# Performance work log

Measured on AMD Instinct MI355X. Metric: run time of the kernel, lower is better.

## Reference

```python
import jax, jax.numpy as jnp
import numpy as np

B, H, W, D = 2, 64, 64, 512
D_HEAD = 64
N_HEADS = D // D_HEAD
KERNEL = 7


def make_neighbourhood_mask(kernel: int, canvas_h: int, canvas_w: int) -> jnp.ndarray:
    """Boolean [HW, HW] mask: query (i,j) attends to a clamped kernel x kernel window."""
    h_ramp = jnp.arange(canvas_h)
    w_ramp = jnp.arange(canvas_w)
    h_pos, w_pos = jnp.meshgrid(h_ramp, w_ramp, indexing='ij')
    start_h = jnp.clip(h_pos - kernel // 2, 0, canvas_h - kernel)[..., None, None]
    end_h = start_h + kernel
    start_w = jnp.clip(w_pos - kernel // 2, 0, canvas_w - kernel)[..., None, None]
    end_w = start_w + kernel
    h_range = h_ramp.reshape(1, 1, canvas_h, 1)
    w_range = w_ramp.reshape(1, 1, 1, canvas_w)
    mask = (h_range >= start_h) & (h_range < end_h) & (w_range >= start_w) & (w_range < end_w)
    return mask.reshape(canvas_h * canvas_w, canvas_h * canvas_w)


def setup_inputs() -> dict:
    key = jax.random.key(0)
    k1, k2, k3 = jax.random.split(key, 3)
    x = jax.random.normal(k1, (B, H, W, D), dtype=jnp.float32)
    w_qkv = jax.random.normal(k2, (3 * D, D), dtype=jnp.float32) * (D ** -0.5)
    w_out = jax.random.normal(k3, (D, D), dtype=jnp.float32) * (D ** -0.5)
    return {"x": x, "w_qkv": w_qkv, "w_out": w_out}


def reference(x, w_qkv, w_out):
    b, h, w, d = x.shape
    s = h * w
    # qkv projection (Linear, no bias): [b,h,w,3d]
    qkv = jnp.einsum('bhwd,ed->bhwe', x, w_qkv)
    # split per torch rearrange 'n h w (t nh e) -> t n nh (h w) e'
    qkv = qkv.reshape(b, s, 3, N_HEADS, D_HEAD).transpose(2, 0, 3, 1, 4)  # [3,b,nh,s,e]
    q, k, v = qkv[0], qkv[1], qkv[2]
    mask = make_neighbourhood_mask(KERNEL, h, w)  # [s, s] bool
    scale = D_HEAD ** -0.5
    scores = jnp.einsum('bnse,bnte->bnst', q, k) * scale  # [b,nh,s,s]
    neg_inf = jnp.finfo(scores.dtype).min
    scores = jnp.where(mask[None, None, :, :], scores, neg_inf)
    attn = jax.nn.softmax(scores, axis=-1)
    out = jnp.einsum('bnst,bnte->bnse', attn, v)  # [b,nh,s,e]
    out = out.transpose(0, 2, 1, 3).reshape(b, h, w, d)  # [b,h,w,d]
    return jnp.einsum('bhwd,ed->bhwe', out, w_out)
```

## Files before the change

### kernel.cpp

```cpp
#include <hip/hip_runtime.h>
#include <hip/hip_bf16.h>


typedef __bf16 bf16x8 __attribute__((ext_vector_type(8)));
typedef __bf16 bf16x4 __attribute__((ext_vector_type(4)));
typedef float  f32x4  __attribute__((ext_vector_type(4)));

__global__ __launch_bounds__(256) void cvt_all(
    const float* __restrict__ x, const float* __restrict__ wq,
    const float* __restrict__ wo, __bf16* __restrict__ xb,
    __bf16* __restrict__ wqb, __bf16* __restrict__ wob) {
  int i = blockIdx.x * 256 + threadIdx.x;
  const float* src;
  __bf16* dst;
  int j = i;
  if (j < 1048576) {
    src = x; dst = xb;
  } else if (j < 1048576 + 196608) {
    j -= 1048576; src = wq; dst = wqb;
  } else {
    j -= 1048576 + 196608; src = wo; dst = wob;
  }
  f32x4 v = ((const f32x4*)src)[j];
  bf16x4 o;
  o[0] = (__bf16)v[0]; o[1] = (__bf16)v[1];
  o[2] = (__bf16)v[2]; o[3] = (__bf16)v[3];
  ((bf16x4*)dst)[j] = o;
}

__device__ __forceinline__ void gload_lds16(const __bf16* g, __bf16* l) {
  __builtin_amdgcn_global_load_lds(
      (const __attribute__((address_space(1))) void*)g,
      (__attribute__((address_space(3))) void*)l, 16, 0, 0);
}

template <bool QKV, int BN>
__global__ __launch_bounds__(256, 3) void gemm_lds(
    const __bf16* __restrict__ A, const __bf16* __restrict__ W,
    __bf16* __restrict__ qo, __bf16* __restrict__ ko, __bf16* __restrict__ vo,
    float* __restrict__ co, int etiles) {
  constexpr int K = 512;
  constexpr int NT = BN / 32;
  __shared__ alignas(16) __bf16 Al[128 * 32];
  __shared__ alignas(16) __bf16 Wl[BN * 32];
  const int tid = threadIdx.x;
  const int wv = tid >> 6, lane = tid & 63;
  const int n16 = lane & 15, quad = lane >> 4;
  const int bi = blockIdx.x / etiles, be = blockIdx.x % etiles;
  const int i0 = bi << 7, e0 = be * BN;
  const int wm = (wv & 1) << 6, we = (wv >> 1) * (BN / 2);

  const int srow = (wv << 4) + (lane >> 2);
  const int scol = (lane & 3) << 3;
  const __bf16* gA = A + (size_t)(i0 + srow) * K + scol;
  const __bf16* gW = W + (size_t)(e0 + srow) * K + scol;
  __bf16* lA = &Al[(wv << 9) + (lane << 3)];
  __bf16* lW = &Wl[(wv << 9) + (lane << 3)];

  f32x4 acc[4][NT];
#pragma unroll
  for (int a = 0; a < 4; ++a)
#pragma unroll
    for (int b = 0; b < NT; ++b) acc[a][b] = (f32x4){0.f, 0.f, 0.f, 0.f};

  for (int k0 = 0; k0 < K; k0 += 32) {
    if (k0) __syncthreads();
    gload_lds16(gA + k0, lA);
    gload_lds16(gA + (size_t)64 * K + k0, lA + 64 * 32);
    gload_lds16(gW + k0, lW);
    if (BN == 128) gload_lds16(gW + (size_t)64 * K + k0, lW + 64 * 32);
    __syncthreads();

    bf16x8 af[4], wf[NT];
#pragma unroll
    for (int t = 0; t < 4; ++t)
      af[t] = *(const bf16x8*)&Al[(wm + t * 16 + n16) * 32 + quad * 8];
#pragma unroll
    for (int t = 0; t < NT; ++t)
      wf[t] = *(const bf16x8*)&Wl[(we + t * 16 + n16) * 32 + quad * 8];
#pragma unroll
    for (int mt = 0; mt < 4; ++mt)
#pragma unroll
      for (int nt = 0; nt < NT; ++nt)
        acc[mt][nt] = __builtin_amdgcn_mfma_f32_16x16x32_bf16(
            af[mt], wf[nt], acc[mt][nt], 0, 0, 0);
  }

#pragma unroll
  for (int mt = 0; mt < 4; ++mt)
#pragma unroll
    for (int nt = 0; nt < NT; ++nt) {
      f32x4 f = acc[mt][nt];
      int e = e0 + we + nt * 16 + n16;
#pragma unroll
      for (int rg = 0; rg < 4; ++rg) {
        int i = i0 + wm + mt * 16 + quad * 4 + rg;
        float val = f[rg];
        if (QKV) {
          int t = e >> 9, head = (e >> 6) & 7, dh = e & 63;
          int b = i >> 12, s = i & 4095;
          int bh = b * 8 + head;
          if (t == 2) {
            vo[((size_t)bh * 64 + dh) * 4096 + s] = (__bf16)val;
          } else {
            size_t off = (((size_t)bh * 4096) + s) * 64 + dh;
            ((t == 0) ? qo : ko)[off] = (__bf16)val;
          }
        } else {
          co[(size_t)i * 512 + e] = val;
        }
      }
    }
}

__global__ __launch_bounds__(256) void attn_mfma(
    const __bf16* __restrict__ q, const __bf16* __restrict__ k,
    const __bf16* __restrict__ vt, __bf16* __restrict__ out) {
  __shared__ alignas(16) __bf16 r1[14848];
  __shared__ alignas(16) __bf16 sbuf[4][16][232];
  const int tid = threadIdx.x;
  const int wv = tid >> 6;
  const int lane = tid & 63;
  const int n16 = lane & 15, quad = lane >> 4;
  const int bh = blockIdx.x >> 6;
  const int tile = blockIdx.x & 63;
  const int qh0 = (tile >> 3) << 3, qw0 = (tile & 7) << 3;
  int wh0 = qh0 - 3; wh0 = wh0 < 0 ? 0 : (wh0 > 50 ? 50 : wh0);
  int wc0 = qw0 - 3; wc0 = wc0 < 0 ? 0 : (wc0 > 48 ? 48 : wc0);
  wc0 &= ~1;
  const size_t base = (size_t)bh * 4096 * 64;

  const int qi_a = wv * 16 + n16;
  const int sqa = (qh0 + (qi_a >> 3)) * 64 + qw0 + (qi_a & 7);
  const __bf16* qp = q + base + (size_t)sqa * 64 + quad * 8;
  bf16x8 aq0 = *(const bf16x8*)qp;
  bf16x8 aq1 = *(const bf16x8*)(qp + 32);

  const __bf16* kbase = k + base;
#pragma unroll
  for (int i = 0; i < 7; ++i) {
    int ch = i * 256 + tid;
    int kr = ch >> 7, wi = ch & 127;
    int kc = wi >> 3, dh8 = wi & 7;
    bf16x8 d = *(const bf16x8*)(kbase +
        (size_t)((wh0 + kr) * 64 + wc0 + kc) * 64 + dh8 * 8);
    *(bf16x8*)&r1[(kr * 16 + kc) * 64 + ((dh8 ^ (kc & 7)) * 8)] = d;
  }
  __syncthreads();

  f32x4 S[14];
  const int skw = wc0 + n16;
  const int sw1 = ((quad ^ (n16 & 7)) * 8);
  const int sw2 = (((4 + quad) ^ (n16 & 7)) * 8);
#pragma unroll
  for (int nt = 0; nt < 14; ++nt) {
    int key = nt * 16 + n16;
    bf16x8 b0 = *(const bf16x8*)&r1[key * 64 + sw1];
    bf16x8 b1 = *(const bf16x8*)&r1[key * 64 + sw2];
    f32x4 s = {0.f, 0.f, 0.f, 0.f};
    s = __builtin_amdgcn_mfma_f32_16x16x32_bf16(aq0, b0, s, 0, 0, 0);
    s = __builtin_amdgcn_mfma_f32_16x16x32_bf16(aq1, b1, s, 0, 0, 0);
    S[nt] = s;
  }

  float mx[4] = {-1e30f, -1e30f, -1e30f, -1e30f};
#pragma unroll
  for (int reg = 0; reg < 4; ++reg) {
    int qi = wv * 16 + quad * 4 + reg;
    int qh = qh0 + (qi >> 3), qw = qw0 + (qi & 7);
    int sh = qh - 3; sh = sh < 0 ? 0 : (sh > 57 ? 57 : sh);
    int sw = qw - 3; sw = sw < 0 ? 0 : (sw > 57 ? 57 : sw);
    bool wok = (skw >= sw) && (skw < sw + 7);
#pragma unroll
    for (int nt = 0; nt < 14; ++nt) {
      int kh = wh0 + nt;
      bool ok = wok && (kh >= sh) && (kh < sh + 7);
      float val = ok ? S[nt][reg] * 0.125f : -1e30f;
      S[nt][reg] = val;
      mx[reg] = mx[reg] > val ? mx[reg] : val;
    }
  }
#pragma unroll
  for (int reg = 0; reg < 4; ++reg)
#pragma unroll
    for (int off = 8; off >= 1; off >>= 1) {
      float o = __shfl_xor(mx[reg], off);
      mx[reg] = mx[reg] > o ? mx[reg] : o;
    }

  float sm[4] = {0.f, 0.f, 0.f, 0.f};
#pragma unroll
  for (int nt = 0; nt < 14; ++nt)
#pragma unroll
    for (int reg = 0; reg < 4; ++reg) {
      float p = __expf(S[nt][reg] - mx[reg]);
      S[nt][reg] = p;
      sm[reg] += p;
    }
#pragma unroll
  for (int reg = 0; reg < 4; ++reg)
#pragma unroll
    for (int off = 8; off >= 1; off >>= 1) sm[reg] += __shfl_xor(sm[reg], off);

#pragma unroll
  for (int reg = 0; reg < 4; ++reg) {
    float inv = 1.f / sm[reg];
    int row = quad * 4 + reg;
#pragma unroll
    for (int nt = 0; nt < 14; ++nt)
      sbuf[wv][row][nt * 16 + n16] = (__bf16)(S[nt][reg] * inv);
  }

  __syncthreads();
  const __bf16* vtb = vt + base;
#pragma unroll
  for (int i = 0; i < 7; ++i) {
    int c = i * 256 + tid;
    int dh = c / 28, rem = c % 28;
    int kr = rem >> 1, half = rem & 1;
    bf16x8 d = *(const bf16x8*)(vtb + (size_t)dh * 4096 +
                                (wh0 + kr) * 64 + wc0 + half * 8);
    *(bf16x8*)&r1[dh * 232 + kr * 16 + half * 8] = d;
  }
  __syncthreads();

  f32x4 O[4] = {{0.f, 0.f, 0.f, 0.f},
                {0.f, 0.f, 0.f, 0.f},
                {0.f, 0.f, 0.f, 0.f},
                {0.f, 0.f, 0.f, 0.f}};
#pragma unroll
  for (int kt = 0; kt < 7; ++kt) {
    bf16x8 pa = *(const bf16x8*)&sbuf[wv][n16][kt * 32 + quad * 8];
    int key0 = kt * 32 + quad * 8;
#pragma unroll
    for (int ntv = 0; ntv < 4; ++ntv) {
      bf16x8 vb = *(const bf16x8*)&r1[(ntv * 16 + n16) * 232 + key0];
      O[ntv] = __builtin_amdgcn_mfma_f32_16x16x32_bf16(pa, vb, O[ntv], 0, 0, 0);
    }
  }

  const int b = bh >> 3, head = bh & 7;
#pragma unroll
  for (int ntv = 0; ntv < 4; ++ntv)
#pragma unroll
    for (int reg = 0; reg < 4; ++reg) {
      int qi = wv * 16 + quad * 4 + reg;
      int s_q = (qh0 + (qi >> 3)) * 64 + qw0 + (qi & 7);
      int dh = ntv * 16 + n16;
      out[((size_t)(b * 4096 + s_q)) * 512 + head * 64 + dh] =
          (__bf16)O[ntv][reg];
    }
}

extern "C" void kernel_launch(void* const* d_in, const int* in_sizes, int n_in,
                              void* d_out, int out_size, void* d_ws,
                              size_t ws_size, hipStream_t stream) {
  const float* x = (const float*)d_in[0];
  const float* w_qkv = (const float*)d_in[1];
  const float* w_out = (const float*)d_in[2];
  float* out = (float*)d_out;

  const size_t qelems = (size_t)2 * 8 * 4096 * 64;
  __bf16* q = (__bf16*)d_ws;
  __bf16* k = q + qelems;
  __bf16* vt = k + qelems;
  __bf16* xb = vt + qelems;
  __bf16* wqb = xb + qelems;
  __bf16* wob = wqb + 1536 * 512;
  __bf16* ao = xb;

  cvt_all<<<dim3(5120), dim3(256), 0, stream>>>(x, w_qkv, w_out, xb, wqb, wob);

  gemm_lds<true, 128><<<dim3(768), dim3(256), 0, stream>>>(
      xb, wqb, q, k, vt, nullptr, 12);
  attn_mfma<<<dim3(1024), dim3(256), 0, stream>>>(q, k, vt, ao);
  gemm_lds<false, 64><<<dim3(512), dim3(256), 0, stream>>>(
      ao, wob, nullptr, nullptr, nullptr, out, 8);
}
```

Before: 137.3 us.

## Split neighborhood attention into single-wave blocks over 2x8 query strips

Replaces the 256-thread attention kernel, where four waves share an 8x8 query tile and a 14-row key window, with one 64-thread wave per 2x8 query strip. Each wave loads its own 8-row K/V window, so there are fewer masked key tiles per query tile (8 instead of 14). The single wave also removes the __syncthreads barriers and waits only on LDS counters. In exchange, overlapping windows are reloaded more often across blocks, the K layout loses its XOR swizzle and may hit LDS bank conflicts, and V is loaded in narrower 4-element chunks.

```diff
diff --git a/kernel.cpp b/kernel.cpp
--- a/kernel.cpp
+++ b/kernel.cpp
@@ -113,50 +113,44 @@
     }
 }
 
-__global__ __launch_bounds__(256) void attn_mfma(
+__global__ __launch_bounds__(64) void attn_wave(
     const __bf16* __restrict__ q, const __bf16* __restrict__ k,
     const __bf16* __restrict__ vt, __bf16* __restrict__ out) {
-  __shared__ alignas(16) __bf16 r1[14848];
-  __shared__ alignas(16) __bf16 sbuf[4][16][232];
-  const int tid = threadIdx.x;
-  const int wv = tid >> 6;
-  const int lane = tid & 63;
+  __shared__ alignas(16) __bf16 kv[8704];
+  __shared__ alignas(16) __bf16 P[16 * 136];
+  const int lane = threadIdx.x;
   const int n16 = lane & 15, quad = lane >> 4;
-  const int bh = blockIdx.x >> 6;
-  const int tile = blockIdx.x & 63;
-  const int qh0 = (tile >> 3) << 3, qw0 = (tile & 7) << 3;
-  int wh0 = qh0 - 3; wh0 = wh0 < 0 ? 0 : (wh0 > 50 ? 50 : wh0);
+  const int bh = blockIdx.x >> 8;
+  const int strip = blockIdx.x & 255;
+  const int qh0 = (strip >> 3) << 1, qw0 = (strip & 7) << 3;
+  int wh0 = qh0 - 3; wh0 = wh0 < 0 ? 0 : (wh0 > 56 ? 56 : wh0);
   int wc0 = qw0 - 3; wc0 = wc0 < 0 ? 0 : (wc0 > 48 ? 48 : wc0);
   wc0 &= ~1;
   const size_t base = (size_t)bh * 4096 * 64;
 
-  const int qi_a = wv * 16 + n16;
-  const int sqa = (qh0 + (qi_a >> 3)) * 64 + qw0 + (qi_a & 7);
+  const int sqa = (qh0 + (n16 >> 3)) * 64 + qw0 + (n16 & 7);
   const __bf16* qp = q + base + (size_t)sqa * 64 + quad * 8;
   bf16x8 aq0 = *(const bf16x8*)qp;
   bf16x8 aq1 = *(const bf16x8*)(qp + 32);
 
   const __bf16* kbase = k + base;
 #pragma unroll
-  for (int i = 0; i < 7; ++i) {
-    int ch = i * 256 + tid;
+  for (int i = 0; i < 16; ++i) {
+    int ch = i * 64 + lane;
     int kr = ch >> 7, wi = ch & 127;
     int kc = wi >> 3, dh8 = wi & 7;
     bf16x8 d = *(const bf16x8*)(kbase +
         (size_t)((wh0 + kr) * 64 + wc0 + kc) * 64 + dh8 * 8);
-    *(bf16x8*)&r1[(kr * 16 + kc) * 64 + ((dh8 ^ (kc & 7)) * 8)] = d;
-  }
-  __syncthreads();
-
-  f32x4 S[14];
+    *(bf16x8*)&kv[(kr * 16 + kc) * 64 + dh8 * 8] = d;
+  }
+
+  f32x4 S[8];
   const int skw = wc0 + n16;
-  const int sw1 = ((quad ^ (n16 & 7)) * 8);
-  const int sw2 = (((4 + quad) ^ (n16 & 7)) * 8);
-#pragma unroll
-  for (int nt = 0; nt < 14; ++nt) {
+#pragma unroll
+  for (int nt = 0; nt < 8; ++nt) {
     int key = nt * 16 + n16;
-    bf16x8 b0 = *(const bf16x8*)&r1[key * 64 + sw1];
-    bf16x8 b1 = *(const bf16x8*)&r1[key * 64 + sw2];
+    bf16x8 b0 = *(const bf16x8*)&kv[key * 64 + quad * 8];
+    bf16x8 b1 = *(const bf16x8*)&kv[key * 64 + 32 + quad * 8];
     f32x4 s = {0.f, 0.f, 0.f, 0.f};
     s = __builtin_amdgcn_mfma_f32_16x16x32_bf16(aq0, b0, s, 0, 0, 0);
     s = __builtin_amdgcn_mfma_f32_16x16x32_bf16(aq1, b1, s, 0, 0, 0);
@@ -166,13 +160,13 @@
   float mx[4] = {-1e30f, -1e30f, -1e30f, -1e30f};
 #pragma unroll
   for (int reg = 0; reg < 4; ++reg) {
-    int qi = wv * 16 + quad * 4 + reg;
+    int qi = quad * 4 + reg;
     int qh = qh0 + (qi >> 3), qw = qw0 + (qi & 7);
     int sh = qh - 3; sh = sh < 0 ? 0 : (sh > 57 ? 57 : sh);
     int sw = qw - 3; sw = sw < 0 ? 0 : (sw > 57 ? 57 : sw);
     bool wok = (skw >= sw) && (skw < sw + 7);
 #pragma unroll
-    for (int nt = 0; nt < 14; ++nt) {
+    for (int nt = 0; nt < 8; ++nt) {
       int kh = wh0 + nt;
       bool ok = wok && (kh >= sh) && (kh < sh + 7);
       float val = ok ? S[nt][reg] * 0.125f : -1e30f;
@@ -190,7 +184,7 @@
 
   float sm[4] = {0.f, 0.f, 0.f, 0.f};
 #pragma unroll
-  for (int nt = 0; nt < 14; ++nt)
+  for (int nt = 0; nt < 8; ++nt)
 #pragma unroll
     for (int reg = 0; reg < 4; ++reg) {
       float p = __expf(S[nt][reg] - mx[reg]);
@@ -207,34 +201,34 @@
     float inv = 1.f / sm[reg];
     int row = quad * 4 + reg;
 #pragma unroll
-    for (int nt = 0; nt < 14; ++nt)
-      sbuf[wv][row][nt * 16 + n16] = (__bf16)(S[nt][reg] * inv);
-  }
-
-  __syncthreads();
+    for (int nt = 0; nt < 8; ++nt)
+      P[row * 136 + nt * 16 + n16] = (__bf16)(S[nt][reg] * inv);
+  }
+
+  asm volatile("s_waitcnt lgkmcnt(0)" ::: "memory");
+
   const __bf16* vtb = vt + base;
 #pragma unroll
-  for (int i = 0; i < 7; ++i) {
-    int c = i * 256 + tid;
-    int dh = c / 28, rem = c % 28;
-    int kr = rem >> 1, half = rem & 1;
-    bf16x8 d = *(const bf16x8*)(vtb + (size_t)dh * 4096 +
-                                (wh0 + kr) * 64 + wc0 + half * 8);
-    *(bf16x8*)&r1[dh * 232 + kr * 16 + half * 8] = d;
-  }
-  __syncthreads();
+  for (int i = 0; i < 32; ++i) {
+    int c = i * 64 + lane;
+    int dh = c >> 5, rem = c & 31;
+    int kr = rem >> 2, qtr = rem & 3;
+    bf16x4 d = *(const bf16x4*)(vtb + (size_t)dh * 4096 +
+                                (wh0 + kr) * 64 + wc0 + qtr * 4);
+    *(bf16x4*)&kv[dh * 136 + kr * 16 + qtr * 4] = d;
+  }
 
   f32x4 O[4] = {{0.f, 0.f, 0.f, 0.f},
                 {0.f, 0.f, 0.f, 0.f},
                 {0.f, 0.f, 0.f, 0.f},
                 {0.f, 0.f, 0.f, 0.f}};
 #pragma unroll
-  for (int kt = 0; kt < 7; ++kt) {
-    bf16x8 pa = *(const bf16x8*)&sbuf[wv][n16][kt * 32 + quad * 8];
+  for (int kt = 0; kt < 4; ++kt) {
+    bf16x8 pa = *(const bf16x8*)&P[n16 * 136 + kt * 32 + quad * 8];
     int key0 = kt * 32 + quad * 8;
 #pragma unroll
     for (int ntv = 0; ntv < 4; ++ntv) {
-      bf16x8 vb = *(const bf16x8*)&r1[(ntv * 16 + n16) * 232 + key0];
+      bf16x8 vb = *(const bf16x8*)&kv[(ntv * 16 + n16) * 136 + key0];
       O[ntv] = __builtin_amdgcn_mfma_f32_16x16x32_bf16(pa, vb, O[ntv], 0, 0, 0);
     }
   }
@@ -244,7 +238,7 @@
   for (int ntv = 0; ntv < 4; ++ntv)
 #pragma unroll
     for (int reg = 0; reg < 4; ++reg) {
-      int qi = wv * 16 + quad * 4 + reg;
+      int qi = quad * 4 + reg;
       int s_q = (qh0 + (qi >> 3)) * 64 + qw0 + (qi & 7);
       int dh = ntv * 16 + n16;
       out[((size_t)(b * 4096 + s_q)) * 512 + head * 64 + dh] =
@@ -273,7 +267,7 @@
 
   gemm_lds<true, 128><<<dim3(768), dim3(256), 0, stream>>>(
       xb, wqb, q, k, vt, nullptr, 12);
-  attn_mfma<<<dim3(1024), dim3(256), 0, stream>>>(q, k, vt, ao);
+  attn_wave<<<dim3(4096), dim3(64), 0, stream>>>(q, k, vt, ao);
   gemm_lds<false, 64><<<dim3(512), dim3(256), 0, stream>>>(
       ao, wob, nullptr, nullptr, nullptr, out, 8);
 }
```

Result: no change. 139.2 us (+1.5%).
